# Optimization experiments

Hardware: AMD Instinct MI355X
Metric: run time of the kernel (lower is better)

The kernel has to match this reference:

```python
import jax, jax.numpy as jnp
import numpy as np

KH = KW = 3  # kernel size for both convs


def conv2d_valid(x, w, b):
    # x: [B,C,H,W], w: [O,C,KH,KW], VALID padding, stride 1 (matches nn.Conv2d(3,18,3))
    y = jax.lax.conv_general_dilated(x, w, window_strides=(1, 1), padding='VALID',
                                     dimension_numbers=('NCHW', 'OIHW', 'NCHW'))
    return y + b[None, :, None, None]


def deform_conv2d(x, offset, w, b):
    # Faithful torchvision deform_conv2d: stride 1, pad 0, dilation 1, 1 group, 1 offset group.
    B, C, H, W = x.shape
    O = w.shape[0]
    Ho, Wo = offset.shape[2], offset.shape[3]
    K = KH * KW
    # offset layout: [B, 2*K, Ho, Wo], per-tap (dy, dx) interleaved, taps row-major
    off = offset.reshape(B, K, 2, Ho, Wo)
    dy, dx = off[:, :, 0], off[:, :, 1]                      # [B,K,Ho,Wo]
    ky = jnp.repeat(jnp.arange(KH), KW).astype(x.dtype)       # [K] tap row
    kx = jnp.tile(jnp.arange(KW), KH).astype(x.dtype)         # [K] tap col
    py = dy + jnp.arange(Ho, dtype=x.dtype)[None, None, :, None] + ky[None, :, None, None]
    px = dx + jnp.arange(Wo, dtype=x.dtype)[None, None, None, :] + kx[None, :, None, None]

    y0 = jnp.floor(py); x0 = jnp.floor(px)
    wy = py - y0; wx = px - x0                                # bilinear fractions
    y0i = y0.astype(jnp.int32); x0i = x0.astype(jnp.int32)

    x_flat = x.reshape(B, C, H * W)

    def corner(yi, xi):
        valid = ((yi >= 0) & (yi < H) & (xi >= 0) & (xi < W)).astype(x.dtype)  # zero pad outside
        idx = jnp.clip(yi, 0, H - 1) * W + jnp.clip(xi, 0, W - 1)              # [B,K,Ho,Wo]
        g = jax.vmap(lambda xf, ix: xf[:, ix])(x_flat, idx)                    # [B,C,K,Ho,Wo]
        return g * valid[:, None]

    val = (corner(y0i, x0i)         * ((1 - wy) * (1 - wx))[:, None]
         + corner(y0i, x0i + 1)     * ((1 - wy) * wx)[:, None]
         + corner(y0i + 1, x0i)     * (wy * (1 - wx))[:, None]
         + corner(y0i + 1, x0i + 1) * (wy * wx)[:, None])     # [B,C,K,Ho,Wo]

    out = jnp.einsum('bckhw,ock->bohw', val, w.reshape(O, C, K))
    return out + b[None, :, None, None]


def setup_inputs() -> dict:
    key = jax.random.key(0)
    k1, k2, k3, k4, k5 = jax.random.split(key, 5)
    B, C, H, W = 16, 3, 384, 384
    x = jax.random.normal(k1, (B, C, H, W), dtype=jnp.float32)
    # offset conv: Conv2d(3, 18, 3); scale down so learned offsets stay moderate
    conv_w = jax.random.normal(k2, (18, 3, KH, KW), dtype=jnp.float32) * 0.05
    conv_b = jax.random.normal(k3, (18,), dtype=jnp.float32) * 0.05
    # deform conv: DeformConv2d(3, 3, 3)
    dcn_w = jax.random.normal(k4, (3, 3, KH, KW), dtype=jnp.float32) * (1.0 / np.sqrt(3 * KH * KW))
    dcn_b = jax.random.normal(k5, (3,), dtype=jnp.float32) * 0.05
    return {'x': x, 'conv_w': conv_w, 'conv_b': conv_b, 'dcn_w': dcn_w, 'dcn_b': dcn_b}


def reference(x, conv_w, conv_b, dcn_w, dcn_b):
    offset = conv2d_valid(x, conv_w, conv_b)   # [B,18,H-2,W-2]
    return deform_conv2d(x, offset, dcn_w, dcn_b)  # [B,3,H-2,W-2]
```

## Files before the change

### kernel.cpp

```cpp
#include <hip/hip_runtime.h>

#define BATCH 16
#define CIN   3
#define H     384
#define W     384
#define HW    (H * W)
#define HO    382
#define WO    382
#define OFFC  18
#define OOUT  3
#define KTAPS 9

#define PAD   2
#define HP    (H + 2 * PAD)
#define WP    (W + 2 * PAD)

#define WPK_FLOATS 588

typedef float vf2 __attribute__((ext_vector_type(2)));
struct F3 { float a, b, c; };

static __device__ __forceinline__ vf2 splat2(float s) { vf2 r; r.x = s; r.y = s; return r; }

static __device__ __forceinline__ unsigned f2bf(float f) {
    const unsigned u = __float_as_uint(f);
    return (u + 0x7fffu + ((u >> 16) & 1u)) >> 16;
}
static __device__ __forceinline__ float bf_lo(unsigned d) { return __uint_as_float(d << 16); }
static __device__ __forceinline__ float bf_hi(unsigned d) { return __uint_as_float(d & 0xffff0000u); }

__global__ __launch_bounds__(256)
void prep_weights_kernel(const float* __restrict__ conv_w,
                         const float* __restrict__ conv_b,
                         const float* __restrict__ dcn_w,
                         const float* __restrict__ dcn_b,
                         float* __restrict__ wpk)
{
    for (int i = threadIdx.x; i < WPK_FLOATS; i += 256) {
        float v;
        if (i < 486) {
            const int k    = i / 54;
            const int r    = i - k * 54;
            const int idx  = r >> 1;
            const int half = r & 1;
            v = conv_w[(2 * k + half) * 27 + idx];
        } else if (i < 504) {
            v = conv_b[i - 486];
        } else if (i < 558) {
            const int r    = i - 504;
            const int ck   = r >> 1;
            const int half = r & 1;
            v = dcn_w[half * 27 + ck];
        } else if (i < 585) {
            v = dcn_w[2 * 27 + (i - 558)];
        } else if (i < 587) {
            v = dcn_b[i - 585];
        } else {
            v = dcn_b[2];
        }
        wpk[i] = v;
    }
}

__global__ __launch_bounds__(256)
void chw_to_bf16hwc_kernel(const float* __restrict__ x, uint2* __restrict__ xt)
{
    const int gid = blockIdx.x * 256 + threadIdx.x;
    if (gid >= BATCH * HP * WP) return;
    const int b  = gid / (HP * WP);
    const int r2 = gid - b * (HP * WP);
    const int ry = r2 / WP;
    const int rx = r2 - ry * WP;
    const int yi = ry - PAD;
    const int xi = rx - PAD;
    uint2 v = make_uint2(0u, 0u);
    if ((unsigned)yi < (unsigned)H && (unsigned)xi < (unsigned)W) {
        const float* xb = x + (size_t)b * (CIN * HW);
        const int p = yi * W + xi;
        v.x = f2bf(xb[p]) | (f2bf(xb[HW + p]) << 16);
        v.y = f2bf(xb[2 * HW + p]);
    }
    xt[gid] = v;
}

__global__ __launch_bounds__(256)
void deform_bf16_kernel(const float* __restrict__ x,
                        const uint2* __restrict__ xt,
                        const float* __restrict__ wpk,
                        float* __restrict__ out)
{
    const int total = BATCH * HO * WO;
    const int gid = blockIdx.x * 256 + threadIdx.x;
    if (gid >= total) return;

    const int wo  = gid % WO;
    const int tmp = gid / WO;
    const int ho  = tmp % HO;
    const int b   = tmp / HO;

    const vf2*   pk_cw = (const vf2*)wpk;
    const vf2*   pk_cb = (const vf2*)(wpk + 486);
    const vf2*   pk_dw = (const vf2*)(wpk + 504);
    const float* dw2   = wpk + 558;

    const float* xb  = x  + (size_t)b * (CIN * HW);
    const uint2* xtb = xt + (size_t)b * (HP * WP);

    float xp[CIN][3][3];
    #pragma unroll
    for (int c = 0; c < CIN; ++c) {
        const float* xc = xb + c * HW + ho * W + wo;
        #pragma unroll
        for (int i = 0; i < 3; ++i)
            #pragma unroll
            for (int j = 0; j < 3; ++j)
                xp[c][i][j] = xc[i * W + j];
    }

    vf2 off2[KTAPS];
    #pragma unroll
    for (int k = 0; k < KTAPS; ++k) {
        vf2 a = pk_cb[k];
        #pragma unroll
        for (int c = 0; c < CIN; ++c)
            #pragma unroll
            for (int i = 0; i < 3; ++i)
                #pragma unroll
                for (int j = 0; j < 3; ++j)
                    a = __builtin_elementwise_fma(pk_cw[k * 27 + c * 9 + i * 3 + j],
                                                  splat2(xp[c][i][j]), a);
        off2[k] = a;
    }

    vf2   acc01 = *(const vf2*)(wpk + 585);
    float acc2  = wpk[587];

    #pragma unroll
    for (int k = 0; k < KTAPS; ++k) {
        const int ky = k / 3;
        const int kx = k % 3;
        const vf2 o = off2[k];
        vf2 f;
        f.x = floorf(o.x);
        f.y = floorf(o.y);
        const vf2 w  = o - f;
        const vf2 cw = splat2(1.f) - w;

        int iy = (int)f.x + (ho + ky + PAD);
        int ix = (int)f.y + (wo + kx + PAD);
        iy = min(max(iy, 0), HP - 2);
        ix = min(max(ix, 0), WP - 2);

        const uint2* base = xtb + iy * WP + ix;
        const uint2 q00 = base[0];
        const uint2 q01 = base[1];
        const uint2 q10 = base[WP];
        const uint2 q11 = base[WP + 1];

        const float w00 = cw.x * cw.y;
        const float w01 = cw.x * w.y;
        const float w10 = w.x * cw.y;
        const float w11 = w.x * w.y;

        vf2 c00, c01, c10, c11;
        c00.x = bf_lo(q00.x); c00.y = bf_hi(q00.x);
        c01.x = bf_lo(q01.x); c01.y = bf_hi(q01.x);
        c10.x = bf_lo(q10.x); c10.y = bf_hi(q10.x);
        c11.x = bf_lo(q11.x); c11.y = bf_hi(q11.x);
        vf2 s01 = c00 * splat2(w00);
        s01 = __builtin_elementwise_fma(c01, splat2(w01), s01);
        s01 = __builtin_elementwise_fma(c10, splat2(w10), s01);
        s01 = __builtin_elementwise_fma(c11, splat2(w11), s01);

        float s2 = bf_lo(q00.y) * w00;
        s2 = fmaf(bf_lo(q01.y), w01, s2);
        s2 = fmaf(bf_lo(q10.y), w10, s2);
        s2 = fmaf(bf_lo(q11.y), w11, s2);

        acc01 = __builtin_elementwise_fma(pk_dw[0 * 9 + k], splat2(s01.x), acc01);
        acc01 = __builtin_elementwise_fma(pk_dw[1 * 9 + k], splat2(s01.y), acc01);
        acc01 = __builtin_elementwise_fma(pk_dw[2 * 9 + k], splat2(s2),    acc01);
        acc2 = fmaf(dw2[0 * 9 + k], s01.x, acc2);
        acc2 = fmaf(dw2[1 * 9 + k], s01.y, acc2);
        acc2 = fmaf(dw2[2 * 9 + k], s2,    acc2);
    }

    const int obase = b * (OOUT * HO * WO) + ho * WO + wo;
    __builtin_nontemporal_store(acc01.x, out + obase);
    __builtin_nontemporal_store(acc01.y, out + obase + HO * WO);
    __builtin_nontemporal_store(acc2,    out + obase + 2 * HO * WO);
}

__global__ __launch_bounds__(256)
void chw_to_hwc_kernel(const float* __restrict__ x, float* __restrict__ xt)
{
    const int gid = blockIdx.x * 256 + threadIdx.x;
    if (gid >= BATCH * HW) return;
    const int b = gid / HW;
    const int p = gid - b * HW;
    const float* xb = x + (size_t)b * (CIN * HW);
    F3 v;
    v.a = xb[p];
    v.b = xb[HW + p];
    v.c = xb[2 * HW + p];
    *(F3*)(xt + (size_t)gid * 3) = v;
}

__global__ __launch_bounds__(256)
void deform_hwc_kernel(const float* __restrict__ xt,
                       const float* __restrict__ conv_w,
                       const float* __restrict__ conv_b,
                       const float* __restrict__ dcn_w,
                       const float* __restrict__ dcn_b,
                       float* __restrict__ out)
{
    const int total = BATCH * HO * WO;
    const int gid = blockIdx.x * 256 + threadIdx.x;
    if (gid >= total) return;

    const int wo  = gid % WO;
    const int tmp = gid / WO;
    const int ho  = tmp % HO;
    const int b   = tmp / HO;

    const float* xtb = xt + (size_t)b * (HW * 3);

    F3 xp[3][3];
    #pragma unroll
    for (int i = 0; i < 3; ++i)
        #pragma unroll
        for (int j = 0; j < 3; ++j)
            xp[i][j] = *(const F3*)(xtb + (size_t)((ho + i) * W + (wo + j)) * 3);

    float off[OFFC];
    #pragma unroll
    for (int o = 0; o < OFFC; ++o) {
        float a = conv_b[o];
        #pragma unroll
        for (int i = 0; i < 3; ++i)
            #pragma unroll
            for (int j = 0; j < 3; ++j) {
                a = fmaf(conv_w[o * 27 + 0 * 9 + i * 3 + j], xp[i][j].a, a);
                a = fmaf(conv_w[o * 27 + 1 * 9 + i * 3 + j], xp[i][j].b, a);
                a = fmaf(conv_w[o * 27 + 2 * 9 + i * 3 + j], xp[i][j].c, a);
            }
        off[o] = a;
    }

    float acc0 = dcn_b[0];
    float acc1 = dcn_b[1];
    float acc2 = dcn_b[2];

    #pragma unroll
    for (int k = 0; k < KTAPS; ++k) {
        const int ky = k / 3;
        const int kx = k % 3;
        const float py = off[2 * k]     + (float)(ho + ky);
        const float px = off[2 * k + 1] + (float)(wo + kx);
        const float y0f = floorf(py);
        const float x0f = floorf(px);
        const float wy = py - y0f;
        const float wx = px - x0f;
        const int y0 = (int)y0f;
        const int x0 = (int)x0f;
        const int y1 = y0 + 1;
        const int x1 = x0 + 1;
        const bool vy0 = (unsigned)y0 < (unsigned)H;
        const bool vy1 = (unsigned)y1 < (unsigned)H;
        const bool vx0 = (unsigned)x0 < (unsigned)W;
        const bool vx1 = (unsigned)x1 < (unsigned)W;
        const int cy0 = min(max(y0, 0), H - 1);
        const int cy1 = min(max(y1, 0), H - 1);
        const int cx0 = min(max(x0, 0), W - 1);
        const int cx1 = min(max(x1, 0), W - 1);
        const float w00 = (vy0 && vx0) ? (1.f - wy) * (1.f - wx) : 0.f;
        const float w01 = (vy0 && vx1) ? (1.f - wy) * wx         : 0.f;
        const float w10 = (vy1 && vx0) ? wy * (1.f - wx)         : 0.f;
        const float w11 = (vy1 && vx1) ? wy * wx                 : 0.f;

        const F3 v00 = *(const F3*)(xtb + (size_t)(cy0 * W + cx0) * 3);
        const F3 v01 = *(const F3*)(xtb + (size_t)(cy0 * W + cx1) * 3);
        const F3 v10 = *(const F3*)(xtb + (size_t)(cy1 * W + cx0) * 3);
        const F3 v11 = *(const F3*)(xtb + (size_t)(cy1 * W + cx1) * 3);

        float s0 = v00.a * w00; s0 = fmaf(v01.a, w01, s0); s0 = fmaf(v10.a, w10, s0); s0 = fmaf(v11.a, w11, s0);
        float s1 = v00.b * w00; s1 = fmaf(v01.b, w01, s1); s1 = fmaf(v10.b, w10, s1); s1 = fmaf(v11.b, w11, s1);
        float s2 = v00.c * w00; s2 = fmaf(v01.c, w01, s2); s2 = fmaf(v10.c, w10, s2); s2 = fmaf(v11.c, w11, s2);

        acc0 = fmaf(dcn_w[0 * 27 + 0 * 9 + k], s0, acc0);
        acc0 = fmaf(dcn_w[0 * 27 + 1 * 9 + k], s1, acc0);
        acc0 = fmaf(dcn_w[0 * 27 + 2 * 9 + k], s2, acc0);
        acc1 = fmaf(dcn_w[1 * 27 + 0 * 9 + k], s0, acc1);
        acc1 = fmaf(dcn_w[1 * 27 + 1 * 9 + k], s1, acc1);
        acc1 = fmaf(dcn_w[1 * 27 + 2 * 9 + k], s2, acc1);
        acc2 = fmaf(dcn_w[2 * 27 + 0 * 9 + k], s0, acc2);
        acc2 = fmaf(dcn_w[2 * 27 + 1 * 9 + k], s1, acc2);
        acc2 = fmaf(dcn_w[2 * 27 + 2 * 9 + k], s2, acc2);
    }

    const int obase = b * (OOUT * HO * WO) + ho * WO + wo;
    __builtin_nontemporal_store(acc0, out + obase);
    __builtin_nontemporal_store(acc1, out + obase + HO * WO);
    __builtin_nontemporal_store(acc2, out + obase + 2 * HO * WO);
}

__global__ __launch_bounds__(256)
void deform_fused_kernel(const float* __restrict__ x,
                         const float* __restrict__ conv_w,
                         const float* __restrict__ conv_b,
                         const float* __restrict__ dcn_w,
                         const float* __restrict__ dcn_b,
                         float* __restrict__ out)
{
    __shared__ float s_cw[OFFC * 27];
    __shared__ float s_cb[OFFC];
    __shared__ float s_dw[OOUT * 27];
    __shared__ float s_db[OOUT];

    const int t = threadIdx.x;
    for (int i = t; i < OFFC * 27; i += 256) s_cw[i] = conv_w[i];
    if (t < OFFC)      s_cb[t] = conv_b[t];
    if (t < OOUT * 27) s_dw[t] = dcn_w[t];
    if (t < OOUT)      s_db[t] = dcn_b[t];
    __syncthreads();

    const int total = BATCH * HO * WO;
    const int gid = blockIdx.x * 256 + t;
    if (gid >= total) return;

    const int wo  = gid % WO;
    const int tmp = gid / WO;
    const int ho  = tmp % HO;
    const int b   = tmp / HO;

    const float* xb = x + b * (CIN * HW);

    float xp[CIN][3][3];
    #pragma unroll
    for (int c = 0; c < CIN; ++c) {
        const float* xc = xb + c * HW + ho * W + wo;
        #pragma unroll
        for (int i = 0; i < 3; ++i)
            #pragma unroll
            for (int j = 0; j < 3; ++j)
                xp[c][i][j] = xc[i * W + j];
    }

    float off[OFFC];
    #pragma unroll
    for (int o = 0; o < OFFC; ++o) {
        float a = s_cb[o];
        const float* wv = &s_cw[o * 27];
        #pragma unroll
        for (int c = 0; c < CIN; ++c)
            #pragma unroll
            for (int i = 0; i < 3; ++i)
                #pragma unroll
                for (int j = 0; j < 3; ++j)
                    a = fmaf(wv[c * 9 + i * 3 + j], xp[c][i][j], a);
        off[o] = a;
    }

    float a0 = s_db[0], a1 = s_db[1], a2 = s_db[2];

    #pragma unroll
    for (int k = 0; k < KTAPS; ++k) {
        const int ky = k / 3;
        const int kx = k % 3;
        const float py = off[2 * k]     + (float)(ho + ky);
        const float px = off[2 * k + 1] + (float)(wo + kx);
        const float y0f = floorf(py);
        const float x0f = floorf(px);
        const float wy = py - y0f;
        const float wx = px - x0f;
        const int y0 = (int)y0f;
        const int x0 = (int)x0f;
        const int y1 = y0 + 1;
        const int x1 = x0 + 1;
        const bool vy0 = (unsigned)y0 < (unsigned)H;
        const bool vy1 = (unsigned)y1 < (unsigned)H;
        const bool vx0 = (unsigned)x0 < (unsigned)W;
        const bool vx1 = (unsigned)x1 < (unsigned)W;
        const int cy0 = min(max(y0, 0), H - 1);
        const int cy1 = min(max(y1, 0), H - 1);
        const int cx0 = min(max(x0, 0), W - 1);
        const int cx1 = min(max(x1, 0), W - 1);
        const float w00 = (vy0 && vx0) ? (1.f - wy) * (1.f - wx) : 0.f;
        const float w01 = (vy0 && vx1) ? (1.f - wy) * wx         : 0.f;
        const float w10 = (vy1 && vx0) ? wy * (1.f - wx)         : 0.f;
        const float w11 = (vy1 && vx1) ? wy * wx                 : 0.f;
        const int i00 = cy0 * W + cx0;
        const int i01 = cy0 * W + cx1;
        const int i10 = cy1 * W + cx0;
        const int i11 = cy1 * W + cx1;
        #pragma unroll
        for (int c = 0; c < CIN; ++c) {
            const float* xc = xb + c * HW;
            float s = xc[i00] * w00;
            s = fmaf(xc[i01], w01, s);
            s = fmaf(xc[i10], w10, s);
            s = fmaf(xc[i11], w11, s);
            a0 = fmaf(s_dw[0 * 27 + c * 9 + k], s, a0);
            a1 = fmaf(s_dw[1 * 27 + c * 9 + k], s, a1);
            a2 = fmaf(s_dw[2 * 27 + c * 9 + k], s, a2);
        }
    }

    const int obase = b * (OOUT * HO * WO) + ho * WO + wo;
    __builtin_nontemporal_store(a0, out + obase);
    __builtin_nontemporal_store(a1, out + obase + HO * WO);
    __builtin_nontemporal_store(a2, out + obase + 2 * HO * WO);
}

extern "C" void kernel_launch(void* const* d_in, const int* in_sizes, int n_in,
                              void* d_out, int out_size, void* d_ws, size_t ws_size,
                              hipStream_t stream) {
    const float* x      = (const float*)d_in[0];
    const float* conv_w = (const float*)d_in[1];
    const float* conv_b = (const float*)d_in[2];
    const float* dcn_w  = (const float*)d_in[3];
    const float* dcn_b  = (const float*)d_in[4];
    float* out = (float*)d_out;

    const int total = BATCH * HO * WO;
    const size_t xt_bytes = (size_t)BATCH * HP * WP * sizeof(uint2);
    const size_t need_bf = xt_bytes + WPK_FLOATS * sizeof(float);
    const size_t need3   = (size_t)BATCH * HW * 3 * sizeof(float);

    if (ws_size >= need_bf) {
        uint2* xt = (uint2*)d_ws;
        float* wpk = (float*)((char*)d_ws + xt_bytes);
        prep_weights_kernel<<<1, 256, 0, stream>>>(conv_w, conv_b, dcn_w, dcn_b, wpk);
        const int cells = BATCH * HP * WP;
        chw_to_bf16hwc_kernel<<<(cells + 255) / 256, 256, 0, stream>>>(x, xt);
        deform_bf16_kernel<<<(total + 255) / 256, 256, 0, stream>>>(x, xt, wpk, out);
    } else if (ws_size >= need3) {
        float* xt = (float*)d_ws;
        chw_to_hwc_kernel<<<(BATCH * HW + 255) / 256, 256, 0, stream>>>(x, xt);
        deform_hwc_kernel<<<(total + 255) / 256, 256, 0, stream>>>(
            xt, conv_w, conv_b, dcn_w, dcn_b, out);
    } else {
        deform_fused_kernel<<<(total + 255) / 256, 256, 0, stream>>>(
            x, conv_w, conv_b, dcn_w, dcn_b, out);
    }
}
```

Before: 147.1 us.

## Pack horizontal pixel pairs into 16-byte bf16 cells for bilinear gathers

```diff
diff --git a/kernel.cpp b/kernel.cpp
--- a/kernel.cpp
+++ b/kernel.cpp
@@ -18,7 +18,6 @@
 #define WPK_FLOATS 588
 
 typedef float vf2 __attribute__((ext_vector_type(2)));
-struct F3 { float a, b, c; };
 
 static __device__ __forceinline__ vf2 splat2(float s) { vf2 r; r.x = s; r.y = s; return r; }
 
@@ -63,6 +62,138 @@
 }
 
 __global__ __launch_bounds__(256)
+void chw_to_cells_kernel(const float* __restrict__ x, uint4* __restrict__ cells)
+{
+    const int gid = blockIdx.x * 256 + threadIdx.x;
+    if (gid >= BATCH * HP * WP) return;
+    const int b  = gid / (HP * WP);
+    const int r2 = gid - b * (HP * WP);
+    const int ry = r2 / WP;
+    const int rx = r2 - ry * WP;
+    const int yi = ry - PAD;
+    const float* xb = x + (size_t)b * (CIN * HW);
+
+    uint4 v = make_uint4(0u, 0u, 0u, 0u);
+    if ((unsigned)yi < (unsigned)H) {
+        const int xiA = rx - PAD;
+        const int xiB = xiA + 1;
+        if ((unsigned)xiA < (unsigned)W) {
+            const int p = yi * W + xiA;
+            v.x = f2bf(xb[p]) | (f2bf(xb[HW + p]) << 16);
+            v.y = f2bf(xb[2 * HW + p]);
+        }
+        if ((unsigned)xiB < (unsigned)W) {
+            const int p = yi * W + xiB;
+            v.z = f2bf(xb[p]) | (f2bf(xb[HW + p]) << 16);
+            v.w = f2bf(xb[2 * HW + p]);
+        }
+    }
+    cells[gid] = v;
+}
+
+__global__ __launch_bounds__(256)
+void deform_cells_kernel(const float* __restrict__ x,
+                         const uint4* __restrict__ cells,
+                         const float* __restrict__ wpk,
+                         float* __restrict__ out)
+{
+    const int p = blockIdx.x * 256 + threadIdx.x;
+    if (p >= HO * WO) return;
+    const int b  = blockIdx.y;
+    const int ho = p / WO;
+    const int wo = p - ho * WO;
+
+    const vf2*   pk_cw = (const vf2*)wpk;
+    const vf2*   pk_cb = (const vf2*)(wpk + 486);
+    const vf2*   pk_dw = (const vf2*)(wpk + 504);
+    const float* dw2   = wpk + 558;
+
+    const float* xb = x     + (size_t)b * (CIN * HW);
+    const uint4* cb = cells + (size_t)b * (HP * WP);
+
+    float xp[CIN][3][3];
+    #pragma unroll
+    for (int c = 0; c < CIN; ++c) {
+        const float* xc = xb + c * HW + ho * W + wo;
+        #pragma unroll
+        for (int i = 0; i < 3; ++i)
+            #pragma unroll
+            for (int j = 0; j < 3; ++j)
+                xp[c][i][j] = xc[i * W + j];
+    }
+
+    vf2 off2[KTAPS];
+    #pragma unroll
+    for (int k = 0; k < KTAPS; ++k) {
+        vf2 a = pk_cb[k];
+        #pragma unroll
+        for (int c = 0; c < CIN; ++c)
+            #pragma unroll
+            for (int i = 0; i < 3; ++i)
+                #pragma unroll
+                for (int j = 0; j < 3; ++j)
+                    a = __builtin_elementwise_fma(pk_cw[k * 27 + c * 9 + i * 3 + j],
+                                                  splat2(xp[c][i][j]), a);
+        off2[k] = a;
+    }
+
+    vf2   acc01 = *(const vf2*)(wpk + 585);
+    float acc2  = wpk[587];
+
+    #pragma unroll
+    for (int k = 0; k < KTAPS; ++k) {
+        const int ky = k / 3;
+        const int kx = k % 3;
+        const vf2 o = off2[k];
+        vf2 f;
+        f.x = floorf(o.x);
+        f.y = floorf(o.y);
+        const vf2 w  = o - f;
+        const vf2 cw = splat2(1.f) - w;
+
+        int iy = (int)f.x + (ho + ky + PAD);
+        int ix = (int)f.y + (wo + kx + PAD);
+        iy = min(max(iy, 0), HP - 2);
+        ix = min(max(ix, 0), WP - 2);
+
+        const int ci = iy * WP + ix;
+        const uint4 c0 = cb[ci];
+        const uint4 c1 = cb[ci + WP];
+
+        vf2 wxv; wxv.x = cw.y; wxv.y = w.y;
+        const vf2 wA = splat2(cw.x) * wxv;
+        const vf2 wB = splat2(w.x)  * wxv;
+
+        vf2 c00, c01, c10, c11;
+        c00.x = bf_lo(c0.x); c00.y = bf_hi(c0.x);
+        c01.x = bf_lo(c0.z); c01.y = bf_hi(c0.z);
+        c10.x = bf_lo(c1.x); c10.y = bf_hi(c1.x);
+        c11.x = bf_lo(c1.z); c11.y = bf_hi(c1.z);
+        vf2 s01 = c00 * splat2(wA.x);
+        s01 = __builtin_elementwise_fma(c01, splat2(wA.y), s01);
+        s01 = __builtin_elementwise_fma(c10, splat2(wB.x), s01);
+        s01 = __builtin_elementwise_fma(c11, splat2(wB.y), s01);
+
+        float s2 = bf_lo(c0.y) * wA.x;
+        s2 = fmaf(bf_lo(c0.w), wA.y, s2);
+        s2 = fmaf(bf_lo(c1.y), wB.x, s2);
+        s2 = fmaf(bf_lo(c1.w), wB.y, s2);
+
+        acc01 = __builtin_elementwise_fma(pk_dw[0 * 9 + k], splat2(s01.x), acc01);
+        acc01 = __builtin_elementwise_fma(pk_dw[1 * 9 + k], splat2(s01.y), acc01);
+        acc01 = __builtin_elementwise_fma(pk_dw[2 * 9 + k], splat2(s2),    acc01);
+        acc2 = fmaf(dw2[0 * 9 + k], s01.x, acc2);
+        acc2 = fmaf(dw2[1 * 9 + k], s01.y, acc2);
+        acc2 = fmaf(dw2[2 * 9 + k], s2,    acc2);
+    }
+
+    const int obase = b * (OOUT * HO * WO) + p;
+    __builtin_nontemporal_store(acc01.x, out + obase);
+    __builtin_nontemporal_store(acc01.y, out + obase + HO * WO);
+    __builtin_nontemporal_store(acc2,    out + obase + 2 * HO * WO);
+}
+
+__global__ __launch_bounds__(256)
 void chw_to_bf16hwc_kernel(const float* __restrict__ x, uint2* __restrict__ xt)
 {
     const int gid = blockIdx.x * 256 + threadIdx.x;
@@ -189,119 +320,6 @@
     __builtin_nontemporal_store(acc01.x, out + obase);
     __builtin_nontemporal_store(acc01.y, out + obase + HO * WO);
     __builtin_nontemporal_store(acc2,    out + obase + 2 * HO * WO);
-}
-
-__global__ __launch_bounds__(256)
-void chw_to_hwc_kernel(const float* __restrict__ x, float* __restrict__ xt)
-{
-    const int gid = blockIdx.x * 256 + threadIdx.x;
-    if (gid >= BATCH * HW) return;
-    const int b = gid / HW;
-    const int p = gid - b * HW;
-    const float* xb = x + (size_t)b * (CIN * HW);
-    F3 v;
-    v.a = xb[p];
-    v.b = xb[HW + p];
-    v.c = xb[2 * HW + p];
-    *(F3*)(xt + (size_t)gid * 3) = v;
-}
-
-__global__ __launch_bounds__(256)
-void deform_hwc_kernel(const float* __restrict__ xt,
-                       const float* __restrict__ conv_w,
-                       const float* __restrict__ conv_b,
-                       const float* __restrict__ dcn_w,
-                       const float* __restrict__ dcn_b,
-                       float* __restrict__ out)
-{
-    const int total = BATCH * HO * WO;
-    const int gid = blockIdx.x * 256 + threadIdx.x;
-    if (gid >= total) return;
-
-    const int wo  = gid % WO;
-    const int tmp = gid / WO;
-    const int ho  = tmp % HO;
-    const int b   = tmp / HO;
-
-    const float* xtb = xt + (size_t)b * (HW * 3);
-
-    F3 xp[3][3];
-    #pragma unroll
-    for (int i = 0; i < 3; ++i)
-        #pragma unroll
-        for (int j = 0; j < 3; ++j)
-            xp[i][j] = *(const F3*)(xtb + (size_t)((ho + i) * W + (wo + j)) * 3);
-
-    float off[OFFC];
-    #pragma unroll
-    for (int o = 0; o < OFFC; ++o) {
-        float a = conv_b[o];
-        #pragma unroll
-        for (int i = 0; i < 3; ++i)
-            #pragma unroll
-            for (int j = 0; j < 3; ++j) {
-                a = fmaf(conv_w[o * 27 + 0 * 9 + i * 3 + j], xp[i][j].a, a);
-                a = fmaf(conv_w[o * 27 + 1 * 9 + i * 3 + j], xp[i][j].b, a);
-                a = fmaf(conv_w[o * 27 + 2 * 9 + i * 3 + j], xp[i][j].c, a);
-            }
-        off[o] = a;
-    }
-
-    float acc0 = dcn_b[0];
-    float acc1 = dcn_b[1];
-    float acc2 = dcn_b[2];
-
-    #pragma unroll
-    for (int k = 0; k < KTAPS; ++k) {
-        const int ky = k / 3;
-        const int kx = k % 3;
-        const float py = off[2 * k]     + (float)(ho + ky);
-        const float px = off[2 * k + 1] + (float)(wo + kx);
-        const float y0f = floorf(py);
-        const float x0f = floorf(px);
-        const float wy = py - y0f;
-        const float wx = px - x0f;
-        const int y0 = (int)y0f;
-        const int x0 = (int)x0f;
-        const int y1 = y0 + 1;
-        const int x1 = x0 + 1;
-        const bool vy0 = (unsigned)y0 < (unsigned)H;
-        const bool vy1 = (unsigned)y1 < (unsigned)H;
-        const bool vx0 = (unsigned)x0 < (unsigned)W;
-        const bool vx1 = (unsigned)x1 < (unsigned)W;
-        const int cy0 = min(max(y0, 0), H - 1);
-        const int cy1 = min(max(y1, 0), H - 1);
-        const int cx0 = min(max(x0, 0), W - 1);
-        const int cx1 = min(max(x1, 0), W - 1);
-        const float w00 = (vy0 && vx0) ? (1.f - wy) * (1.f - wx) : 0.f;
-        const float w01 = (vy0 && vx1) ? (1.f - wy) * wx         : 0.f;
-        const float w10 = (vy1 && vx0) ? wy * (1.f - wx)         : 0.f;
-        const float w11 = (vy1 && vx1) ? wy * wx                 : 0.f;
-
-        const F3 v00 = *(const F3*)(xtb + (size_t)(cy0 * W + cx0) * 3);
-        const F3 v01 = *(const F3*)(xtb + (size_t)(cy0 * W + cx1) * 3);
-        const F3 v10 = *(const F3*)(xtb + (size_t)(cy1 * W + cx0) * 3);
-        const F3 v11 = *(const F3*)(xtb + (size_t)(cy1 * W + cx1) * 3);
-
-        float s0 = v00.a * w00; s0 = fmaf(v01.a, w01, s0); s0 = fmaf(v10.a, w10, s0); s0 = fmaf(v11.a, w11, s0);
-        float s1 = v00.b * w00; s1 = fmaf(v01.b, w01, s1); s1 = fmaf(v10.b, w10, s1); s1 = fmaf(v11.b, w11, s1);
-        float s2 = v00.c * w00; s2 = fmaf(v01.c, w01, s2); s2 = fmaf(v10.c, w10, s2); s2 = fmaf(v11.c, w11, s2);
-
-        acc0 = fmaf(dcn_w[0 * 27 + 0 * 9 + k], s0, acc0);
-        acc0 = fmaf(dcn_w[0 * 27 + 1 * 9 + k], s1, acc0);
-        acc0 = fmaf(dcn_w[0 * 27 + 2 * 9 + k], s2, acc0);
-        acc1 = fmaf(dcn_w[1 * 27 + 0 * 9 + k], s0, acc1);
-        acc1 = fmaf(dcn_w[1 * 27 + 1 * 9 + k], s1, acc1);
-        acc1 = fmaf(dcn_w[1 * 27 + 2 * 9 + k], s2, acc1);
-        acc2 = fmaf(dcn_w[2 * 27 + 0 * 9 + k], s0, acc2);
-        acc2 = fmaf(dcn_w[2 * 27 + 1 * 9 + k], s1, acc2);
-        acc2 = fmaf(dcn_w[2 * 27 + 2 * 9 + k], s2, acc2);
-    }
-
-    const int obase = b * (OOUT * HO * WO) + ho * WO + wo;
-    __builtin_nontemporal_store(acc0, out + obase);
-    __builtin_nontemporal_store(acc1, out + obase + HO * WO);
-    __builtin_nontemporal_store(acc2, out + obase + 2 * HO * WO);
 }
 
 __global__ __launch_bounds__(256)
@@ -423,22 +441,26 @@
     float* out = (float*)d_out;
 
     const int total = BATCH * HO * WO;
-    const size_t xt_bytes = (size_t)BATCH * HP * WP * sizeof(uint2);
-    const size_t need_bf = xt_bytes + WPK_FLOATS * sizeof(float);
-    const size_t need3   = (size_t)BATCH * HW * 3 * sizeof(float);
-
-    if (ws_size >= need_bf) {
+    const size_t cells_bytes = (size_t)BATCH * HP * WP * sizeof(uint4);
+    const size_t need_cells  = cells_bytes + WPK_FLOATS * sizeof(float);
+    const size_t xt_bytes    = (size_t)BATCH * HP * WP * sizeof(uint2);
+    const size_t need_bf     = xt_bytes + WPK_FLOATS * sizeof(float);
+
+    if (ws_size >= need_cells) {
+        uint4* cells = (uint4*)d_ws;
+        float* wpk = (float*)((char*)d_ws + cells_bytes);
+        prep_weights_kernel<<<1, 256, 0, stream>>>(conv_w, conv_b, dcn_w, dcn_b, wpk);
+        const int nc = BATCH * HP * WP;
+        chw_to_cells_kernel<<<(nc + 255) / 256, 256, 0, stream>>>(x, cells);
+        dim3 grid((HO * WO + 255) / 256, BATCH, 1);
+        deform_cells_kernel<<<grid, 256, 0, stream>>>(x, cells, wpk, out);
+    } else if (ws_size >= need_bf) {
         uint2* xt = (uint2*)d_ws;
         float* wpk = (float*)((char*)d_ws + xt_bytes);
         prep_weights_kernel<<<1, 256, 0, stream>>>(conv_w, conv_b, dcn_w, dcn_b, wpk);
-        const int cells = BATCH * HP * WP;
-        chw_to_bf16hwc_kernel<<<(cells + 255) / 256, 256, 0, stream>>>(x, xt);
+        const int nc = BATCH * HP * WP;
+        chw_to_bf16hwc_kernel<<<(nc + 255) / 256, 256, 0, stream>>>(x, xt);
         deform_bf16_kernel<<<(total + 255) / 256, 256, 0, stream>>>(x, xt, wpk, out);
-    } else if (ws_size >= need3) {
-        float* xt = (float*)d_ws;
-        chw_to_hwc_kernel<<<(BATCH * HW + 255) / 256, 256, 0, stream>>>(x, xt);
-        deform_hwc_kernel<<<(total + 255) / 256, 256, 0, stream>>>(
-            xt, conv_w, conv_b, dcn_w, dcn_b, out);
     } else {
         deform_fused_kernel<<<(total + 255) / 256, 256, 0, stream>>>(
             x, conv_w, conv_b, dcn_w, dcn_b, out);
```

Result: no change. 147.2 us (+0.1%).
